# Performance work log

Hardware: AMD Instinct MI355X
Metric: run time of the kernel (lower is better)

Reference implementation:

```python
import jax, jax.numpy as jnp
import numpy as np

N_NODES = 20000
N_EDGES = 40000
MAX_NB = 6
N_ATOM_FEAT = 98
N_BOND_FEAT = 13
HIDDEN = 256
DEPTH = 4
INPUT_SIZE = N_ATOM_FEAT + N_BOND_FEAT  # 111, hmess width


def setup_inputs() -> dict:
    key = jax.random.key(0)
    ks = jax.random.split(key, 10)
    fnode = jax.random.normal(ks[0], (N_NODES, N_ATOM_FEAT), jnp.float32)
    # fmess: col0/col1 are src/dst node indices stored as floats, cols 2: are bond features
    idx = jax.random.randint(ks[1], (N_EDGES, 2), 0, N_NODES).astype(jnp.float32)
    bond = jax.random.normal(ks[2], (N_EDGES, N_BOND_FEAT), jnp.float32)
    fmess = jnp.concatenate([idx, bond], axis=1)  # [E, 2 + n_bond_feat]
    agraph = jax.random.randint(ks[3], (N_NODES, MAX_NB), 0, N_EDGES)
    bgraph = jax.random.randint(ks[4], (N_EDGES, MAX_NB), 0, N_EDGES)
    s = 0.02
    W_z_w = jax.random.normal(ks[5], (HIDDEN, INPUT_SIZE + HIDDEN), jnp.float32) * s
    W_z_b = jnp.zeros((HIDDEN,), jnp.float32)
    W_r_w = jax.random.normal(ks[6], (HIDDEN, INPUT_SIZE), jnp.float32) * s  # no bias (W_r)
    U_r_w = jax.random.normal(ks[7], (HIDDEN, HIDDEN), jnp.float32) * s
    U_r_b = jnp.zeros((HIDDEN,), jnp.float32)
    W_h_w = jax.random.normal(ks[8], (HIDDEN, INPUT_SIZE + HIDDEN), jnp.float32) * s
    W_h_b = jnp.zeros((HIDDEN,), jnp.float32)
    W_o_w = jax.random.normal(ks[9], (HIDDEN, N_ATOM_FEAT + HIDDEN), jnp.float32) * s
    W_o_b = jnp.zeros((HIDDEN,), jnp.float32)
    return dict(fnode=fnode, fmess=fmess, agraph=agraph, bgraph=bgraph,
                W_z_w=W_z_w, W_z_b=W_z_b, W_r_w=W_r_w, U_r_w=U_r_w, U_r_b=U_r_b,
                W_h_w=W_h_w, W_h_b=W_h_b, W_o_w=W_o_w, W_o_b=W_o_b)


def reference(fnode, fmess, agraph, bgraph,
              W_z_w, W_z_b, W_r_w, U_r_w, U_r_b, W_h_w, W_h_b, W_o_w, W_o_b):
    # GraphFeatEncoder: gather src-node features and concat with bond features
    src = fmess[:, 0].astype(jnp.int32)
    x = jnp.concatenate([fnode[src], fmess[:, 2:]], axis=-1)  # [E, input_size]
    E = x.shape[0]
    H = W_z_b.shape[0]
    emask = jnp.ones((E, 1), x.dtype).at[0, 0].set(0.0)  # message 0 is padding
    Wr_x = (x @ W_r_w.T)[:, None, :]  # [E,1,H], constant across depth iterations
    h = jnp.zeros((E, H), x.dtype)
    # DGCNGRU: D-MPNN style GRU over directed-edge states
    for _ in range(DEPTH):
        h_nei = h[bgraph]                                   # [E, max_nb, H] gather
        sum_h = h_nei.sum(axis=1)                           # [E, H]
        z = jax.nn.sigmoid(jnp.concatenate([x, sum_h], axis=1) @ W_z_w.T + W_z_b)
        r = jax.nn.sigmoid(Wr_x + h_nei @ U_r_w.T + U_r_b)  # [E, max_nb, H]
        sum_gh = (r * h_nei).sum(axis=1)
        pre_h = jnp.tanh(jnp.concatenate([x, sum_gh], axis=1) @ W_h_w.T + W_h_b)
        h = ((1.0 - z) * sum_h + z * pre_h) * emask
    # DGCNEncoder readout: aggregate incoming edge states per atom
    nei_msg = h[agraph].sum(axis=1)                          # [N, H] gather + sum
    node_h = jax.nn.gelu(jnp.concatenate([fnode, nei_msg], axis=1) @ W_o_w.T + W_o_b,
                         approximate=False)                  # torch nn.GELU = exact erf
    nmask = jnp.ones((node_h.shape[0], 1), node_h.dtype).at[0, 0].set(0.0)  # node 0 pad
    hatom = node_h * nmask
    return hatom  # GraphFeatEncoder returns (hatom, None); hmol is always None
```

## Files before the change

kernel.cpp:

```cpp
#include <hip/hip_runtime.h>
#include <cstddef>
#include <cstdint>

typedef unsigned short u16;
typedef unsigned int   u32;
typedef __bf16  bf16x8 __attribute__((ext_vector_type(8)));
typedef float   f32x4  __attribute__((ext_vector_type(4)));

#define DEV __device__ __forceinline__

DEV float b2f(u16 u) { union { u32 i; float f; } c; c.i = ((u32)u) << 16; return c.f; }
DEV u16 f2b(float x) { union { float f; u32 i; } c; c.f = x; u32 b = c.i;
                       return (u16)((b + 0x7FFFu + ((b >> 16) & 1u)) >> 16); }
DEV float sigm(float x)  { return 1.0f / (1.0f + __expf(-x)); }
DEV float tanh_(float x) { return 1.0f - 2.0f / (1.0f + __expf(2.0f * x)); }
DEV float gelu_(float x) { return 0.5f * x * (1.0f + erff(x * 0.70710678118654752f)); }

DEV void u4tof8(uint4 v, float* f) {
    f[0] = b2f((u16)(v.x & 0xFFFF)); f[1] = b2f((u16)(v.x >> 16));
    f[2] = b2f((u16)(v.y & 0xFFFF)); f[3] = b2f((u16)(v.y >> 16));
    f[4] = b2f((u16)(v.z & 0xFFFF)); f[5] = b2f((u16)(v.z >> 16));
    f[6] = b2f((u16)(v.w & 0xFFFF)); f[7] = b2f((u16)(v.w >> 16));
}
DEV uint4 f8tou4(const float* f) {
    uint4 v;
    v.x = (u32)f2b(f[0]) | ((u32)f2b(f[1]) << 16);
    v.y = (u32)f2b(f[2]) | ((u32)f2b(f[3]) << 16);
    v.z = (u32)f2b(f[4]) | ((u32)f2b(f[5]) << 16);
    v.w = (u32)f2b(f[6]) | ((u32)f2b(f[7]) << 16);
    return v;
}

#define OB_PRU   0ull
#define OB_PZX   20480000ull
#define OB_PHX   40960000ull
#define OB_H     61440000ull
#define OB_UH    81920000ull
#define OB_SH    102400000ull
#define OB_SGH   122880000ull
#define OB_BZX   143360000ull
#define OB_BZH   143425536ull
#define OB_BHX   143556608ull
#define OB_BHH   143622144ull
#define OB_BU    143753216ull
#define OB_BOH   143884288ull
#define OB_BR    OB_UH
#define OB_BOX   (OB_UH + 65536ull)
#define WS_BYTES 144015360ull


DEV int xcd_swz(int bid, int nwg) {
    int q = nwg >> 3, r = nwg & 7;
    int xcd = bid & 7, idx = bid >> 3;
    return (xcd < r ? xcd * (q + 1) : r * (q + 1) + (xcd - r) * q) + idx;
}

__global__ __launch_bounds__(256) void k_repack(
    const float* __restrict__ Wz, const float* __restrict__ Wr,
    const float* __restrict__ Ur, const float* __restrict__ Wh,
    const float* __restrict__ Wo,
    u16* __restrict__ BzxT, u16* __restrict__ BzhT, u16* __restrict__ BhxT,
    u16* __restrict__ BhhT, u16* __restrict__ BuT, u16* __restrict__ BohT,
    u16* __restrict__ BrT, u16* __restrict__ BoxT) {
    int idx = blockIdx.x * 256 + threadIdx.x;
    {
        int n = idx >> 8, k = idx & 255;
        BzhT[idx] = f2b(Wz[n * 367 + 111 + k]);
        BhhT[idx] = f2b(Wh[n * 367 + 111 + k]);
        BuT[idx]  = f2b(Ur[idx]);
        BohT[idx] = f2b(Wo[n * 354 + 98 + k]);
    }
    if (idx < 32768) {
        int n = idx >> 7, k = idx & 127;
        BzxT[idx] = f2b(k < 111 ? Wz[n * 367 + k] : 0.0f);
        BhxT[idx] = f2b(k < 111 ? Wh[n * 367 + k] : 0.0f);
        BrT[idx]  = f2b(k < 111 ? Wr[n * 111 + k] : 0.0f);
        BoxT[idx] = f2b(k < 98  ? Wo[n * 354 + k] : 0.0f);
    }
}

__global__ __launch_bounds__(256) void k_build_x(const float* __restrict__ fnode,
                                                 const float* __restrict__ fmess,
                                                 u16* __restrict__ x) {
    int e = (blockIdx.x << 1) + (threadIdx.x >> 7);
    int c = threadIdx.x & 127;
    int src = (int)fmess[(size_t)e * 15];
    float v = 0.0f;
    if (c < 98)       v = fnode[(size_t)src * 98 + c];
    else if (c < 111) v = fmess[(size_t)e * 15 + 2 + (c - 98)];
    x[(size_t)e * 128 + c] = f2b(v);
}

__global__ __launch_bounds__(256) void k_build_fb(const float* __restrict__ fnode,
                                                  u16* __restrict__ fb) {
    int idx = blockIdx.x * 256 + threadIdx.x;
    int n = idx >> 7, c = idx & 127;
    fb[idx] = f2b(c < 98 ? fnode[(size_t)n * 98 + c] : 0.0f);
}

DEV void ldA(const u16* __restrict__ g, size_t row0, int ld, int k0, int tid, uint4* v) {
    #pragma unroll
    for (int it = 0; it < 4; ++it) {
        int r = it * 32 + (tid >> 3);
        int c = (tid & 7) << 3;
        v[it] = *(const uint4*)(g + (row0 + (size_t)r) * ld + k0 + c);
    }
}
DEV void ldB(const u16* __restrict__ g, size_t row0, int ld, int k0, int tid, uint4* v) {
    #pragma unroll
    for (int it = 0; it < 2; ++it) {
        int r = it * 32 + (tid >> 3);
        int c = (tid & 7) << 3;
        v[it] = *(const uint4*)(g + (row0 + (size_t)r) * ld + k0 + c);
    }
}
DEV void wrA(u16* s, int tid, const uint4* v) {
    #pragma unroll
    for (int it = 0; it < 4; ++it) {
        int r = it * 32 + (tid >> 3);
        int c = (tid & 7) << 3;
        int byte = (((r << 6) + c) << 1) ^ ((r & 7) << 4);
        *(uint4*)((char*)s + byte) = v[it];
    }
}
DEV void wrB(u16* s, int tid, const uint4* v) {
    #pragma unroll
    for (int it = 0; it < 2; ++it) {
        int r = it * 32 + (tid >> 3);
        int c = (tid & 7) << 3;
        int byte = (((r << 6) + c) << 1) ^ ((r & 7) << 4);
        *(uint4*)((char*)s + byte) = v[it];
    }
}
DEV void mma_step(const u16* As, const u16* Bs, f32x4 acc[4][2], int lane, int wr, int wc) {
    int rb = (wr << 6) + (lane & 15);
    int cb = (wc << 5) + (lane & 15);
    int ko = (lane >> 4) << 3;
    #pragma unroll
    for (int kh = 0; kh < 2; ++kh) {
        bf16x8 a[4], b[2];
        #pragma unroll
        for (int i = 0; i < 4; ++i) {
            int ar = rb + (i << 4);
            a[i] = *(const bf16x8*)((const char*)As +
                   ((((ar << 6) + (kh << 5) + ko) << 1) ^ ((ar & 7) << 4)));
        }
        #pragma unroll
        for (int j = 0; j < 2; ++j) {
            int br = cb + (j << 4);
            b[j] = *(const bf16x8*)((const char*)Bs +
                   ((((br << 6) + (kh << 5) + ko) << 1) ^ ((br & 7) << 4)));
        }
        #pragma unroll
        for (int i = 0; i < 4; ++i)
            #pragma unroll
            for (int j = 0; j < 2; ++j)
                acc[i][j] = __builtin_amdgcn_mfma_f32_16x16x32_bf16(b[j], a[i], acc[i][j], 0, 0, 0);
    }
}

#define GT_PROLOG()                                            \
    int tid = threadIdx.x, lane = tid & 63, w = tid >> 6;      \
    int wr = w >> 1, wc = w & 1;                               \
    int bid = xcd_swz((int)blockIdx.x, (int)gridDim.x);        \
    int bm = bid >> 2, bn = bid & 3;                           \
    size_t m0 = (size_t)bm << 7; size_t n0 = (size_t)(bn << 6);\
    int row_l = (wr << 6) + (lane & 15);                       \
    int col_l = (wc << 5) + ((lane >> 4) << 2);

#define ACC_INIT(A)                                            \
    { f32x4 zz = {0.f, 0.f, 0.f, 0.f};                         \
      _Pragma("unroll") for (int i = 0; i < 4; ++i)            \
      _Pragma("unroll") for (int j = 0; j < 2; ++j) A[i][j] = zz; }

#define DB_STEP(CUR_A, CUR_B, NXT_A, NXT_B, LD_NEXT2)          \
    mma_step(CUR_A, CUR_B, acc, lane, wr, wc);                 \
    wrA(NXT_A, tid, ra); wrB(NXT_B, tid, rb);                  \
    __syncthreads();                                           \
    LD_NEXT2;

__global__ __launch_bounds__(256) void k_mg_k128(
    const u16* __restrict__ A, const u16* __restrict__ BT,
    const float* __restrict__ bias, u16* __restrict__ out) {
    __shared__ u16 As0[8192], As1[8192], Bs0[4096], Bs1[4096];
    GT_PROLOG()
    f32x4 acc[4][2]; ACC_INIT(acc)
    uint4 ra[4], rb[2];
    ldA(A, m0, 128, 0, tid, ra); ldB(BT, n0, 128, 0, tid, rb);
    wrA(As0, tid, ra); wrB(Bs0, tid, rb);
    __syncthreads();
    ldA(A, m0, 128, 64, tid, ra); ldB(BT, n0, 128, 64, tid, rb);
    DB_STEP(As0, Bs0, As1, Bs1, ;)
    mma_step(As1, Bs1, acc, lane, wr, wc);
    #pragma unroll
    for (int mi = 0; mi < 4; ++mi) {
        int m = (int)m0 + row_l + (mi << 4);
        if (m >= 40000) continue;
        #pragma unroll
        for (int ni = 0; ni < 2; ++ni) {
            int col = (int)n0 + col_l + (ni << 4);
            float4 ub = bias ? *(const float4*)(bias + col)
                             : make_float4(0.f, 0.f, 0.f, 0.f);
            ushort4 o;
            o.x = f2b(acc[mi][ni][0] + ub.x); o.y = f2b(acc[mi][ni][1] + ub.y);
            o.z = f2b(acc[mi][ni][2] + ub.z); o.w = f2b(acc[mi][ni][3] + ub.w);
            *(ushort4*)(out + (size_t)m * 256 + col) = o;
        }
    }
}

__global__ __launch_bounds__(256) void k_mg_pn(
    const u16* __restrict__ fb, const u16* __restrict__ BT,
    float* __restrict__ out) {
    __shared__ u16 As0[8192], As1[8192], Bs0[4096], Bs1[4096];
    GT_PROLOG()
    f32x4 acc[4][2]; ACC_INIT(acc)
    uint4 ra[4], rb[2];
    ldA(fb, m0, 128, 0, tid, ra); ldB(BT, n0, 128, 0, tid, rb);
    wrA(As0, tid, ra); wrB(Bs0, tid, rb);
    __syncthreads();
    ldA(fb, m0, 128, 64, tid, ra); ldB(BT, n0, 128, 64, tid, rb);
    DB_STEP(As0, Bs0, As1, Bs1, ;)
    mma_step(As1, Bs1, acc, lane, wr, wc);
    #pragma unroll
    for (int mi = 0; mi < 4; ++mi) {
        int m = (int)m0 + row_l + (mi << 4);
        if (m >= 20000) continue;
        #pragma unroll
        for (int ni = 0; ni < 2; ++ni) {
            int col = (int)n0 + col_l + (ni << 4);
            #pragma unroll
            for (int q = 0; q < 4; ++q)
                out[(size_t)m * 256 + col + q] = acc[mi][ni][q];
        }
    }
}

__global__ __launch_bounds__(256) void k_d1(
    const u16* __restrict__ Pzx, const u16* __restrict__ Phx,
    const float* __restrict__ bz, const float* __restrict__ bh,
    u16* __restrict__ h) {
    int idx = blockIdx.x * 256 + threadIdx.x;
    int e = idx >> 5, c = (idx & 31) << 3;
    size_t o = (size_t)e * 256 + c;
    float pz[8], ph[8], r[8];
    u4tof8(*(const uint4*)(Pzx + o), pz);
    u4tof8(*(const uint4*)(Phx + o), ph);
    #pragma unroll
    for (int q = 0; q < 8; ++q)
        r[q] = (e == 0) ? 0.0f : sigm(pz[q] + bz[c + q]) * tanh_(ph[q] + bh[c + q]);
    *(uint4*)(h + o) = f8tou4(r);
}

__global__ __launch_bounds__(256) void k_mg_uh(
    const u16* __restrict__ A, const u16* __restrict__ BT, u16* __restrict__ C) {
    __shared__ u16 As0[8192], As1[8192], Bs0[4096], Bs1[4096];
    GT_PROLOG()
    f32x4 acc[4][2]; ACC_INIT(acc)
    uint4 ra[4], rb[2];
    ldA(A, m0, 256, 0, tid, ra); ldB(BT, n0, 256, 0, tid, rb);
    wrA(As0, tid, ra); wrB(Bs0, tid, rb);
    __syncthreads();
    ldA(A, m0, 256, 64, tid, ra); ldB(BT, n0, 256, 64, tid, rb);
    DB_STEP(As0, Bs0, As1, Bs1, (ldA(A, m0, 256, 128, tid, ra), ldB(BT, n0, 256, 128, tid, rb)))
    DB_STEP(As1, Bs1, As0, Bs0, (ldA(A, m0, 256, 192, tid, ra), ldB(BT, n0, 256, 192, tid, rb)))
    DB_STEP(As0, Bs0, As1, Bs1, ;)
    mma_step(As1, Bs1, acc, lane, wr, wc);
    #pragma unroll
    for (int mi = 0; mi < 4; ++mi) {
        int m = (int)m0 + row_l + (mi << 4);
        if (m >= 40000) continue;
        #pragma unroll
        for (int ni = 0; ni < 2; ++ni) {
            int col = (int)n0 + col_l + (ni << 4);
            ushort4 o;
            o.x = f2b(acc[mi][ni][0]); o.y = f2b(acc[mi][ni][1]);
            o.z = f2b(acc[mi][ni][2]); o.w = f2b(acc[mi][ni][3]);
            *(ushort4*)(C + (size_t)m * 256 + col) = o;
        }
    }
}

__global__ __launch_bounds__(256) void k_mg_z(
    const u16* __restrict__ sumh, const u16* __restrict__ BT,
    const u16* __restrict__ Pzx, const float* __restrict__ bz,
    u16* __restrict__ zb) {
    __shared__ u16 As0[8192], As1[8192], Bs0[4096], Bs1[4096];
    GT_PROLOG()
    f32x4 acc[4][2]; ACC_INIT(acc)
    uint4 ra[4], rb[2];
    ldA(sumh, m0, 256, 0, tid, ra); ldB(BT, n0, 256, 0, tid, rb);
    wrA(As0, tid, ra); wrB(Bs0, tid, rb);
    __syncthreads();
    ldA(sumh, m0, 256, 64, tid, ra); ldB(BT, n0, 256, 64, tid, rb);
    DB_STEP(As0, Bs0, As1, Bs1, (ldA(sumh, m0, 256, 128, tid, ra), ldB(BT, n0, 256, 128, tid, rb)))
    DB_STEP(As1, Bs1, As0, Bs0, (ldA(sumh, m0, 256, 192, tid, ra), ldB(BT, n0, 256, 192, tid, rb)))
    DB_STEP(As0, Bs0, As1, Bs1, ;)
    mma_step(As1, Bs1, acc, lane, wr, wc);
    #pragma unroll
    for (int mi = 0; mi < 4; ++mi) {
        int m = (int)m0 + row_l + (mi << 4);
        if (m >= 40000) continue;
        #pragma unroll
        for (int ni = 0; ni < 2; ++ni) {
            int col = (int)n0 + col_l + (ni << 4);
            float4 vz = *(const float4*)(bz + col);
            ushort4 p4 = *(const ushort4*)(Pzx + (size_t)m * 256 + col);
            ushort4 o;
            o.x = f2b(sigm(acc[mi][ni][0] + b2f(p4.x) + vz.x));
            o.y = f2b(sigm(acc[mi][ni][1] + b2f(p4.y) + vz.y));
            o.z = f2b(sigm(acc[mi][ni][2] + b2f(p4.z) + vz.z));
            o.w = f2b(sigm(acc[mi][ni][3] + b2f(p4.w) + vz.w));
            *(ushort4*)(zb + (size_t)m * 256 + col) = o;
        }
    }
}

__global__ __launch_bounds__(256) void k_mg_h(
    const u16* __restrict__ sumgh, const u16* __restrict__ BT,
    const u16* __restrict__ Phx, const float* __restrict__ bh,
    const u16* __restrict__ zb, const u16* __restrict__ sumh,
    u16* __restrict__ h) {
    __shared__ u16 As0[8192], As1[8192], Bs0[4096], Bs1[4096];
    GT_PROLOG()
    f32x4 acc[4][2]; ACC_INIT(acc)
    uint4 ra[4], rb[2];
    ldA(sumgh, m0, 256, 0, tid, ra); ldB(BT, n0, 256, 0, tid, rb);
    wrA(As0, tid, ra); wrB(Bs0, tid, rb);
    __syncthreads();
    ldA(sumgh, m0, 256, 64, tid, ra); ldB(BT, n0, 256, 64, tid, rb);
    DB_STEP(As0, Bs0, As1, Bs1, (ldA(sumgh, m0, 256, 128, tid, ra), ldB(BT, n0, 256, 128, tid, rb)))
    DB_STEP(As1, Bs1, As0, Bs0, (ldA(sumgh, m0, 256, 192, tid, ra), ldB(BT, n0, 256, 192, tid, rb)))
    DB_STEP(As0, Bs0, As1, Bs1, ;)
    mma_step(As1, Bs1, acc, lane, wr, wc);
    #pragma unroll
    for (int mi = 0; mi < 4; ++mi) {
        int m = (int)m0 + row_l + (mi << 4);
        if (m >= 40000) continue;
        #pragma unroll
        for (int ni = 0; ni < 2; ++ni) {
            int col = (int)n0 + col_l + (ni << 4);
            float4 vh = *(const float4*)(bh + col);
            ushort4 p4  = *(const ushort4*)(Phx  + (size_t)m * 256 + col);
            ushort4 z4  = *(const ushort4*)(zb   + (size_t)m * 256 + col);
            ushort4 sh4 = *(const ushort4*)(sumh + (size_t)m * 256 + col);
            float pv[4]  = {b2f(p4.x),  b2f(p4.y),  b2f(p4.z),  b2f(p4.w)};
            float zv[4]  = {b2f(z4.x),  b2f(z4.y),  b2f(z4.z),  b2f(z4.w)};
            float shv[4] = {b2f(sh4.x), b2f(sh4.y), b2f(sh4.z), b2f(sh4.w)};
            float bhv[4] = {vh.x, vh.y, vh.z, vh.w};
            float o[4];
            #pragma unroll
            for (int q = 0; q < 4; ++q) {
                float pre = tanh_(acc[mi][ni][q] + pv[q] + bhv[q]);
                o[q] = (1.0f - zv[q]) * shv[q] + zv[q] * pre;
            }
            if (m == 0) { o[0] = o[1] = o[2] = o[3] = 0.0f; }
            ushort4 ov;
            ov.x = f2b(o[0]); ov.y = f2b(o[1]); ov.z = f2b(o[2]); ov.w = f2b(o[3]);
            *(ushort4*)(h + (size_t)m * 256 + col) = ov;
        }
    }
}

__global__ __launch_bounds__(256) void k_mg_out(
    const u16* __restrict__ nei, const u16* __restrict__ BT,
    const float* __restrict__ bo, float* __restrict__ out) {
    __shared__ u16 As0[8192], As1[8192], Bs0[4096], Bs1[4096];
    GT_PROLOG()
    f32x4 acc[4][2]; ACC_INIT(acc)
    uint4 ra[4], rb[2];
    ldA(nei, m0, 256, 0, tid, ra); ldB(BT, n0, 256, 0, tid, rb);
    wrA(As0, tid, ra); wrB(Bs0, tid, rb);
    __syncthreads();
    ldA(nei, m0, 256, 64, tid, ra); ldB(BT, n0, 256, 64, tid, rb);
    DB_STEP(As0, Bs0, As1, Bs1, (ldA(nei, m0, 256, 128, tid, ra), ldB(BT, n0, 256, 128, tid, rb)))
    DB_STEP(As1, Bs1, As0, Bs0, (ldA(nei, m0, 256, 192, tid, ra), ldB(BT, n0, 256, 192, tid, rb)))
    DB_STEP(As0, Bs0, As1, Bs1, ;)
    mma_step(As1, Bs1, acc, lane, wr, wc);
    #pragma unroll
    for (int mi = 0; mi < 4; ++mi) {
        int m = (int)m0 + row_l + (mi << 4);
        if (m >= 20000) continue;
        #pragma unroll
        for (int ni = 0; ni < 2; ++ni) {
            int col = (int)n0 + col_l + (ni << 4);
            float4 vb = *(const float4*)(bo + col);
            const float bv[4] = {vb.x, vb.y, vb.z, vb.w};
            float o[4];
            #pragma unroll
            for (int q = 0; q < 4; ++q) {
                float pn = out[(size_t)m * 256 + col + q];
                o[q] = (m == 0) ? 0.0f : gelu_(acc[mi][ni][q] + pn + bv[q]);
            }
            #pragma unroll
            for (int q = 0; q < 4; ++q)
                out[(size_t)m * 256 + col + q] = o[q];
        }
    }
}

__global__ __launch_bounds__(256) void k_gather_edge(
    const u16* __restrict__ h, const u16* __restrict__ Uh,
    const u16* __restrict__ PrU, const int* __restrict__ bgraph,
    u16* __restrict__ sumh, u16* __restrict__ sumgh) {
    int e = (blockIdx.x << 3) + (threadIdx.x >> 5);
    int c = (threadIdx.x & 31) << 3;
    size_t o = (size_t)e * 256 + c;
    int bi[6];
    *(int2*)&bi[0] = *(const int2*)(bgraph + e * 6 + 0);
    *(int2*)&bi[2] = *(const int2*)(bgraph + e * 6 + 2);
    *(int2*)&bi[4] = *(const int2*)(bgraph + e * 6 + 4);
    float pr[8];
    u4tof8(*(const uint4*)(PrU + o), pr);
    float sh[8] = {}, sg[8] = {};
    uint4 hv4 = *(const uint4*)(h  + (size_t)bi[0] * 256 + c);
    uint4 uv4 = *(const uint4*)(Uh + (size_t)bi[0] * 256 + c);
    #pragma unroll
    for (int j = 0; j < 6; ++j) {
        uint4 hn, un;
        if (j < 5) {
            hn = *(const uint4*)(h  + (size_t)bi[j + 1] * 256 + c);
            un = *(const uint4*)(Uh + (size_t)bi[j + 1] * 256 + c);
        }
        float hv[8], uv[8];
        u4tof8(hv4, hv); u4tof8(uv4, uv);
        #pragma unroll
        for (int q = 0; q < 8; ++q) {
            sh[q] += hv[q];
            sg[q] += sigm(pr[q] + uv[q]) * hv[q];
        }
        hv4 = hn; uv4 = un;
    }
    *(uint4*)(sumh  + o) = f8tou4(sh);
    *(uint4*)(sumgh + o) = f8tou4(sg);
}

__global__ __launch_bounds__(256) void k_gather_node(
    const u16* __restrict__ h, const int* __restrict__ agraph,
    u16* __restrict__ nei) {
    int n = (blockIdx.x << 3) + (threadIdx.x >> 5);
    int c = (threadIdx.x & 31) << 3;
    int ai[6];
    *(int2*)&ai[0] = *(const int2*)(agraph + n * 6 + 0);
    *(int2*)&ai[2] = *(const int2*)(agraph + n * 6 + 2);
    *(int2*)&ai[4] = *(const int2*)(agraph + n * 6 + 4);
    float s[8] = {};
    uint4 hv4 = *(const uint4*)(h + (size_t)ai[0] * 256 + c);
    #pragma unroll
    for (int j = 0; j < 6; ++j) {
        uint4 hn;
        if (j < 5) hn = *(const uint4*)(h + (size_t)ai[j + 1] * 256 + c);
        float hv[8];
        u4tof8(hv4, hv);
        #pragma unroll
        for (int q = 0; q < 8; ++q) s[q] += hv[q];
        hv4 = hn;
    }
    *(uint4*)(nei + (size_t)n * 256 + c) = f8tou4(s);
}

extern "C" void kernel_launch(void* const* d_in, const int* in_sizes, int n_in,
                              void* d_out, int out_size, void* d_ws, size_t ws_size,
                              hipStream_t stream) {
    if (ws_size < WS_BYTES) return;

    const float* fnode  = (const float*)d_in[0];
    const float* fmess  = (const float*)d_in[1];
    const int*   agraph = (const int*)d_in[2];
    const int*   bgraph = (const int*)d_in[3];
    const float* Wz  = (const float*)d_in[4];
    const float* bz  = (const float*)d_in[5];
    const float* Wr  = (const float*)d_in[6];
    const float* Ur  = (const float*)d_in[7];
    const float* urb = (const float*)d_in[8];
    const float* Wh  = (const float*)d_in[9];
    const float* bh  = (const float*)d_in[10];
    const float* Wo  = (const float*)d_in[11];
    const float* bo  = (const float*)d_in[12];

    char* base = (char*)d_ws;
    u16* PrU   = (u16*)(base + OB_PRU);
    u16* Pzx   = (u16*)(base + OB_PZX);
    u16* Phx   = (u16*)(base + OB_PHX);
    u16* h     = (u16*)(base + OB_H);
    u16* Uh    = (u16*)(base + OB_UH);
    u16* zb    = (u16*)(base + OB_UH);
    u16* nei   = (u16*)(base + OB_UH);
    u16* sumh  = (u16*)(base + OB_SH);
    u16* x     = (u16*)(base + OB_SH);
    u16* sumgh = (u16*)(base + OB_SGH);
    u16* fb    = (u16*)(base + OB_SGH);
    u16* BzxT  = (u16*)(base + OB_BZX);
    u16* BzhT  = (u16*)(base + OB_BZH);
    u16* BhxT  = (u16*)(base + OB_BHX);
    u16* BhhT  = (u16*)(base + OB_BHH);
    u16* BuT   = (u16*)(base + OB_BU);
    u16* BohT  = (u16*)(base + OB_BOH);
    u16* BrT   = (u16*)(base + OB_BR);
    u16* BoxT  = (u16*)(base + OB_BOX);
    float* out = (float*)d_out;

    hipLaunchKernelGGL(k_repack, dim3(256), dim3(256), 0, stream,
                       Wz, Wr, Ur, Wh, Wo, BzxT, BzhT, BhxT, BhhT, BuT, BohT, BrT, BoxT);
    hipLaunchKernelGGL(k_build_x, dim3(20000), dim3(256), 0, stream, fnode, fmess, x);
    hipLaunchKernelGGL(k_build_fb, dim3(10000), dim3(256), 0, stream, fnode, fb);
    hipLaunchKernelGGL(k_mg_k128, dim3(1252), dim3(256), 0, stream, x, BrT, urb, PrU);
    hipLaunchKernelGGL(k_mg_k128, dim3(1252), dim3(256), 0, stream, x, BzxT, (const float*)0, Pzx);
    hipLaunchKernelGGL(k_mg_k128, dim3(1252), dim3(256), 0, stream, x, BhxT, (const float*)0, Phx);
    hipLaunchKernelGGL(k_mg_pn, dim3(628), dim3(256), 0, stream, fb, BoxT, out);
    hipLaunchKernelGGL(k_d1, dim3(5000), dim3(256), 0, stream, Pzx, Phx, bz, bh, h);
    for (int d = 1; d < 4; ++d) {
        hipLaunchKernelGGL(k_mg_uh, dim3(1252), dim3(256), 0, stream, h, BuT, Uh);
        hipLaunchKernelGGL(k_gather_edge, dim3(5000), dim3(256), 0, stream,
                           h, Uh, PrU, bgraph, sumh, sumgh);
        hipLaunchKernelGGL(k_mg_z, dim3(1252), dim3(256), 0, stream,
                           sumh, BzhT, Pzx, bz, zb);
        hipLaunchKernelGGL(k_mg_h, dim3(1252), dim3(256), 0, stream,
                           sumgh, BhhT, Phx, bh, zb, sumh, h);
    }
    hipLaunchKernelGGL(k_gather_node, dim3(2500), dim3(256), 0, stream, h, agraph, nei);
    hipLaunchKernelGGL(k_mg_out, dim3(628), dim3(256), 0, stream, nei, BohT, bo, out);
}
```

Before: 444.1 us.

## Fuse z and h GEMMs per tile and merge three precompute GEMMs

The z-gate GEMM and the h-candidate GEMM now run in one kernel. The z tile is kept in swizzled shared memory instead of being written to and reread from a global zb buffer. The three K=128 precompute GEMMs are also batched into a single launch with 3x the grid, selecting weights and outputs by block index. This removes one global round trip of z and several launches, at the cost of an extra 16 KB of LDS per block, which may lower occupancy.

```diff
diff --git a/kernel.cpp b/kernel.cpp
--- a/kernel.cpp
+++ b/kernel.cpp
@@ -159,10 +159,10 @@
     }
 }
 
-#define GT_PROLOG()                                            \
+#define GT_PROLOG(BIDX, NWG)                                   \
     int tid = threadIdx.x, lane = tid & 63, w = tid >> 6;      \
     int wr = w >> 1, wc = w & 1;                               \
-    int bid = xcd_swz((int)blockIdx.x, (int)gridDim.x);        \
+    int bid = xcd_swz((BIDX), (NWG));                          \
     int bm = bid >> 2, bn = bid & 3;                           \
     size_t m0 = (size_t)bm << 7; size_t n0 = (size_t)(bn << 6);\
     int row_l = (wr << 6) + (lane & 15);                       \
@@ -179,17 +179,24 @@
     __syncthreads();                                           \
     LD_NEXT2;
 
-__global__ __launch_bounds__(256) void k_mg_k128(
-    const u16* __restrict__ A, const u16* __restrict__ BT,
-    const float* __restrict__ bias, u16* __restrict__ out) {
+__global__ __launch_bounds__(256) void k_mg_pre(
+    const u16* __restrict__ x, const u16* __restrict__ BrT,
+    const u16* __restrict__ BzxT, const u16* __restrict__ BhxT,
+    const float* __restrict__ urb,
+    u16* __restrict__ PrU, u16* __restrict__ Pzx, u16* __restrict__ Phx) {
     __shared__ u16 As0[8192], As1[8192], Bs0[4096], Bs1[4096];
-    GT_PROLOG()
+    int sub = blockIdx.x / 1252;
+    int inner = blockIdx.x - sub * 1252;
+    const u16* BT = sub == 0 ? BrT : (sub == 1 ? BzxT : BhxT);
+    const float* bias = sub == 0 ? urb : (const float*)0;
+    u16* out = sub == 0 ? PrU : (sub == 1 ? Pzx : Phx);
+    GT_PROLOG(inner, 1252)
     f32x4 acc[4][2]; ACC_INIT(acc)
     uint4 ra[4], rb[2];
-    ldA(A, m0, 128, 0, tid, ra); ldB(BT, n0, 128, 0, tid, rb);
+    ldA(x, m0, 128, 0, tid, ra); ldB(BT, n0, 128, 0, tid, rb);
     wrA(As0, tid, ra); wrB(Bs0, tid, rb);
     __syncthreads();
-    ldA(A, m0, 128, 64, tid, ra); ldB(BT, n0, 128, 64, tid, rb);
+    ldA(x, m0, 128, 64, tid, ra); ldB(BT, n0, 128, 64, tid, rb);
     DB_STEP(As0, Bs0, As1, Bs1, ;)
     mma_step(As1, Bs1, acc, lane, wr, wc);
     #pragma unroll
@@ -213,7 +220,7 @@
     const u16* __restrict__ fb, const u16* __restrict__ BT,
     float* __restrict__ out) {
     __shared__ u16 As0[8192], As1[8192], Bs0[4096], Bs1[4096];
-    GT_PROLOG()
+    GT_PROLOG((int)blockIdx.x, (int)gridDim.x)
     f32x4 acc[4][2]; ACC_INIT(acc)
     uint4 ra[4], rb[2];
     ldA(fb, m0, 128, 0, tid, ra); ldB(BT, n0, 128, 0, tid, rb);
@@ -255,7 +262,7 @@
 __global__ __launch_bounds__(256) void k_mg_uh(
     const u16* __restrict__ A, const u16* __restrict__ BT, u16* __restrict__ C) {
     __shared__ u16 As0[8192], As1[8192], Bs0[4096], Bs1[4096];
-    GT_PROLOG()
+    GT_PROLOG((int)blockIdx.x, (int)gridDim.x)
     f32x4 acc[4][2]; ACC_INIT(acc)
     uint4 ra[4], rb[2];
     ldA(A, m0, 256, 0, tid, ra); ldB(BT, n0, 256, 0, tid, rb);
@@ -281,83 +288,87 @@
     }
 }
 
-__global__ __launch_bounds__(256) void k_mg_z(
-    const u16* __restrict__ sumh, const u16* __restrict__ BT,
-    const u16* __restrict__ Pzx, const float* __restrict__ bz,
-    u16* __restrict__ zb) {
-    __shared__ u16 As0[8192], As1[8192], Bs0[4096], Bs1[4096];
-    GT_PROLOG()
-    f32x4 acc[4][2]; ACC_INIT(acc)
-    uint4 ra[4], rb[2];
-    ldA(sumh, m0, 256, 0, tid, ra); ldB(BT, n0, 256, 0, tid, rb);
-    wrA(As0, tid, ra); wrB(Bs0, tid, rb);
-    __syncthreads();
-    ldA(sumh, m0, 256, 64, tid, ra); ldB(BT, n0, 256, 64, tid, rb);
-    DB_STEP(As0, Bs0, As1, Bs1, (ldA(sumh, m0, 256, 128, tid, ra), ldB(BT, n0, 256, 128, tid, rb)))
-    DB_STEP(As1, Bs1, As0, Bs0, (ldA(sumh, m0, 256, 192, tid, ra), ldB(BT, n0, 256, 192, tid, rb)))
-    DB_STEP(As0, Bs0, As1, Bs1, ;)
-    mma_step(As1, Bs1, acc, lane, wr, wc);
-    #pragma unroll
-    for (int mi = 0; mi < 4; ++mi) {
-        int m = (int)m0 + row_l + (mi << 4);
-        if (m >= 40000) continue;
-        #pragma unroll
-        for (int ni = 0; ni < 2; ++ni) {
-            int col = (int)n0 + col_l + (ni << 4);
-            float4 vz = *(const float4*)(bz + col);
-            ushort4 p4 = *(const ushort4*)(Pzx + (size_t)m * 256 + col);
-            ushort4 o;
-            o.x = f2b(sigm(acc[mi][ni][0] + b2f(p4.x) + vz.x));
-            o.y = f2b(sigm(acc[mi][ni][1] + b2f(p4.y) + vz.y));
-            o.z = f2b(sigm(acc[mi][ni][2] + b2f(p4.z) + vz.z));
-            o.w = f2b(sigm(acc[mi][ni][3] + b2f(p4.w) + vz.w));
-            *(ushort4*)(zb + (size_t)m * 256 + col) = o;
-        }
-    }
-}
-
-__global__ __launch_bounds__(256) void k_mg_h(
-    const u16* __restrict__ sumgh, const u16* __restrict__ BT,
-    const u16* __restrict__ Phx, const float* __restrict__ bh,
-    const u16* __restrict__ zb, const u16* __restrict__ sumh,
+__global__ __launch_bounds__(256) void k_mg_zh(
+    const u16* __restrict__ sumh, const u16* __restrict__ sumgh,
+    const u16* __restrict__ BzhT, const u16* __restrict__ BhhT,
+    const u16* __restrict__ Pzx, const u16* __restrict__ Phx,
+    const float* __restrict__ bz, const float* __restrict__ bh,
     u16* __restrict__ h) {
     __shared__ u16 As0[8192], As1[8192], Bs0[4096], Bs1[4096];
-    GT_PROLOG()
-    f32x4 acc[4][2]; ACC_INIT(acc)
+    __shared__ u16 Zs[8192];
+    GT_PROLOG((int)blockIdx.x, (int)gridDim.x)
     uint4 ra[4], rb[2];
-    ldA(sumgh, m0, 256, 0, tid, ra); ldB(BT, n0, 256, 0, tid, rb);
-    wrA(As0, tid, ra); wrB(Bs0, tid, rb);
+    {
+        f32x4 acc[4][2]; ACC_INIT(acc)
+        ldA(sumh, m0, 256, 0, tid, ra); ldB(BzhT, n0, 256, 0, tid, rb);
+        wrA(As0, tid, ra); wrB(Bs0, tid, rb);
+        __syncthreads();
+        ldA(sumh, m0, 256, 64, tid, ra); ldB(BzhT, n0, 256, 64, tid, rb);
+        DB_STEP(As0, Bs0, As1, Bs1, (ldA(sumh, m0, 256, 128, tid, ra), ldB(BzhT, n0, 256, 128, tid, rb)))
+        DB_STEP(As1, Bs1, As0, Bs0, (ldA(sumh, m0, 256, 192, tid, ra), ldB(BzhT, n0, 256, 192, tid, rb)))
+        DB_STEP(As0, Bs0, As1, Bs1, ;)
+        mma_step(As1, Bs1, acc, lane, wr, wc);
+        #pragma unroll
+        for (int mi = 0; mi < 4; ++mi) {
+            int m = (int)m0 + row_l + (mi << 4);
+            if (m >= 40000) continue;
+            #pragma unroll
+            for (int ni = 0; ni < 2; ++ni) {
+                int col = (int)n0 + col_l + (ni << 4);
+                float4 vz = *(const float4*)(bz + col);
+                ushort4 p4 = *(const ushort4*)(Pzx + (size_t)m * 256 + col);
+                ushort4 o;
+                o.x = f2b(sigm(acc[mi][ni][0] + b2f(p4.x) + vz.x));
+                o.y = f2b(sigm(acc[mi][ni][1] + b2f(p4.y) + vz.y));
+                o.z = f2b(sigm(acc[mi][ni][2] + b2f(p4.z) + vz.z));
+                o.w = f2b(sigm(acc[mi][ni][3] + b2f(p4.w) + vz.w));
+                int rr = row_l + (mi << 4);
+                int cc = col_l + (ni << 4);
+                int byte = (((rr << 6) + cc) << 1) ^ ((rr & 7) << 4);
+                *(ushort4*)((char*)Zs + byte) = o;
+            }
+        }
+    }
     __syncthreads();
-    ldA(sumgh, m0, 256, 64, tid, ra); ldB(BT, n0, 256, 64, tid, rb);
-    DB_STEP(As0, Bs0, As1, Bs1, (ldA(sumgh, m0, 256, 128, tid, ra), ldB(BT, n0, 256, 128, tid, rb)))
-    DB_STEP(As1, Bs1, As0, Bs0, (ldA(sumgh, m0, 256, 192, tid, ra), ldB(BT, n0, 256, 192, tid, rb)))
-    DB_STEP(As0, Bs0, As1, Bs1, ;)
-    mma_step(As1, Bs1, acc, lane, wr, wc);
-    #pragma unroll
-    for (int mi = 0; mi < 4; ++mi) {
-        int m = (int)m0 + row_l + (mi << 4);
-        if (m >= 40000) continue;
-        #pragma unroll
-        for (int ni = 0; ni < 2; ++ni) {
-            int col = (int)n0 + col_l + (ni << 4);
-            float4 vh = *(const float4*)(bh + col);
-            ushort4 p4  = *(const ushort4*)(Phx  + (size_t)m * 256 + col);
-            ushort4 z4  = *(const ushort4*)(zb   + (size_t)m * 256 + col);
-            ushort4 sh4 = *(const ushort4*)(sumh + (size_t)m * 256 + col);
-            float pv[4]  = {b2f(p4.x),  b2f(p4.y),  b2f(p4.z),  b2f(p4.w)};
-            float zv[4]  = {b2f(z4.x),  b2f(z4.y),  b2f(z4.z),  b2f(z4.w)};
-            float shv[4] = {b2f(sh4.x), b2f(sh4.y), b2f(sh4.z), b2f(sh4.w)};
-            float bhv[4] = {vh.x, vh.y, vh.z, vh.w};
-            float o[4];
+    {
+        f32x4 acc[4][2]; ACC_INIT(acc)
+        ldA(sumgh, m0, 256, 0, tid, ra); ldB(BhhT, n0, 256, 0, tid, rb);
+        wrA(As0, tid, ra); wrB(Bs0, tid, rb);
+        __syncthreads();
+        ldA(sumgh, m0, 256, 64, tid, ra); ldB(BhhT, n0, 256, 64, tid, rb);
+        DB_STEP(As0, Bs0, As1, Bs1, (ldA(sumgh, m0, 256, 128, tid, ra), ldB(BhhT, n0, 256, 128, tid, rb)))
+        DB_STEP(As1, Bs1, As0, Bs0, (ldA(sumgh, m0, 256, 192, tid, ra), ldB(BhhT, n0, 256, 192, tid, rb)))
+        DB_STEP(As0, Bs0, As1, Bs1, ;)
+        mma_step(As1, Bs1, acc, lane, wr, wc);
+        #pragma unroll
+        for (int mi = 0; mi < 4; ++mi) {
+            int m = (int)m0 + row_l + (mi << 4);
+            if (m >= 40000) continue;
             #pragma unroll
-            for (int q = 0; q < 4; ++q) {
-                float pre = tanh_(acc[mi][ni][q] + pv[q] + bhv[q]);
-                o[q] = (1.0f - zv[q]) * shv[q] + zv[q] * pre;
+            for (int ni = 0; ni < 2; ++ni) {
+                int col = (int)n0 + col_l + (ni << 4);
+                float4 vh = *(const float4*)(bh + col);
+                ushort4 p4  = *(const ushort4*)(Phx  + (size_t)m * 256 + col);
+                ushort4 sh4 = *(const ushort4*)(sumh + (size_t)m * 256 + col);
+                int rr = row_l + (mi << 4);
+                int cc = col_l + (ni << 4);
+                int byte = (((rr << 6) + cc) << 1) ^ ((rr & 7) << 4);
+                ushort4 z4 = *(const ushort4*)((const char*)Zs + byte);
+                float pv[4]  = {b2f(p4.x),  b2f(p4.y),  b2f(p4.z),  b2f(p4.w)};
+                float zv[4]  = {b2f(z4.x),  b2f(z4.y),  b2f(z4.z),  b2f(z4.w)};
+                float shv[4] = {b2f(sh4.x), b2f(sh4.y), b2f(sh4.z), b2f(sh4.w)};
+                float bhv[4] = {vh.x, vh.y, vh.z, vh.w};
+                float o[4];
+                #pragma unroll
+                for (int q = 0; q < 4; ++q) {
+                    float pre = tanh_(acc[mi][ni][q] + pv[q] + bhv[q]);
+                    o[q] = (1.0f - zv[q]) * shv[q] + zv[q] * pre;
+                }
+                if (m == 0) { o[0] = o[1] = o[2] = o[3] = 0.0f; }
+                ushort4 ov;
+                ov.x = f2b(o[0]); ov.y = f2b(o[1]); ov.z = f2b(o[2]); ov.w = f2b(o[3]);
+                *(ushort4*)(h + (size_t)m * 256 + col) = ov;
             }
-            if (m == 0) { o[0] = o[1] = o[2] = o[3] = 0.0f; }
-            ushort4 ov;
-            ov.x = f2b(o[0]); ov.y = f2b(o[1]); ov.z = f2b(o[2]); ov.w = f2b(o[3]);
-            *(ushort4*)(h + (size_t)m * 256 + col) = ov;
         }
     }
 }
@@ -366,7 +377,7 @@
     const u16* __restrict__ nei, const u16* __restrict__ BT,
     const float* __restrict__ bo, float* __restrict__ out) {
     __shared__ u16 As0[8192], As1[8192], Bs0[4096], Bs1[4096];
-    GT_PROLOG()
+    GT_PROLOG((int)blockIdx.x, (int)gridDim.x)
     f32x4 acc[4][2]; ACC_INIT(acc)
     uint4 ra[4], rb[2];
     ldA(nei, m0, 256, 0, tid, ra); ldB(BT, n0, 256, 0, tid, rb);
@@ -484,7 +495,6 @@
     u16* Phx   = (u16*)(base + OB_PHX);
     u16* h     = (u16*)(base + OB_H);
     u16* Uh    = (u16*)(base + OB_UH);
-    u16* zb    = (u16*)(base + OB_UH);
     u16* nei   = (u16*)(base + OB_UH);
     u16* sumh  = (u16*)(base + OB_SH);
     u16* x     = (u16*)(base + OB_SH);
@@ -504,19 +514,16 @@
                        Wz, Wr, Ur, Wh, Wo, BzxT, BzhT, BhxT, BhhT, BuT, BohT, BrT, BoxT);
     hipLaunchKernelGGL(k_build_x, dim3(20000), dim3(256), 0, stream, fnode, fmess, x);
     hipLaunchKernelGGL(k_build_fb, dim3(10000), dim3(256), 0, stream, fnode, fb);
-    hipLaunchKernelGGL(k_mg_k128, dim3(1252), dim3(256), 0, stream, x, BrT, urb, PrU);
-    hipLaunchKernelGGL(k_mg_k128, dim3(1252), dim3(256), 0, stream, x, BzxT, (const float*)0, Pzx);
-    hipLaunchKernelGGL(k_mg_k128, dim3(1252), dim3(256), 0, stream, x, BhxT, (const float*)0, Phx);
+    hipLaunchKernelGGL(k_mg_pre, dim3(3756), dim3(256), 0, stream,
+                       x, BrT, BzxT, BhxT, urb, PrU, Pzx, Phx);
     hipLaunchKernelGGL(k_mg_pn, dim3(628), dim3(256), 0, stream, fb, BoxT, out);
     hipLaunchKernelGGL(k_d1, dim3(5000), dim3(256), 0, stream, Pzx, Phx, bz, bh, h);
     for (int d = 1; d < 4; ++d) {
         hipLaunchKernelGGL(k_mg_uh, dim3(1252), dim3(256), 0, stream, h, BuT, Uh);
         hipLaunchKernelGGL(k_gather_edge, dim3(5000), dim3(256), 0, stream,
                            h, Uh, PrU, bgraph, sumh, sumgh);
-        hipLaunchKernelGGL(k_mg_z, dim3(1252), dim3(256), 0, stream,
-                           sumh, BzhT, Pzx, bz, zb);
-        hipLaunchKernelGGL(k_mg_h, dim3(1252), dim3(256), 0, stream,
-                           sumgh, BhhT, Phx, bh, zb, sumh, h);
+        hipLaunchKernelGGL(k_mg_zh, dim3(1252), dim3(256), 0, stream,
+                           sumh, sumgh, BzhT, BhhT, Pzx, Phx, bz, bh, h);
     }
     hipLaunchKernelGGL(k_gather_node, dim3(2500), dim3(256), 0, stream, h, agraph, nei);
     hipLaunchKernelGGL(k_mg_out, dim3(628), dim3(256), 0, stream, nei, BohT, bo, out);
```

After: 426.6 us, median of 2. 1.04x faster.
